# Performance work log

Measured on AMD Instinct MI355X. Metric: run time of the kernel, lower is better.

## Reference

```python
import jax, jax.numpy as jnp
import numpy as np

N, E, D, L = 50000, 600000, 128, 3
EPS = 1e-5


def _layer_norm(x, g, b):
    m = jnp.mean(x, axis=-1, keepdims=True)
    v = jnp.mean((x - m) ** 2, axis=-1, keepdims=True)
    return (x - m) * jax.lax.rsqrt(v + EPS) * g + b


def setup_inputs() -> dict:
    key = jax.random.key(0)
    ks = jax.random.split(key, 20)
    s = 1.0 / np.sqrt(D)
    inp = {
        "node": jax.random.normal(ks[0], (N, D), jnp.float32),
        "edge_attr": jax.random.uniform(ks[1], (E,), jnp.float32),
        # stacked per-layer parameters [L, ...]
        "W_rel": jax.random.uniform(ks[2], (L, D, D), jnp.float32, -s, s),
        "b_rel": jax.random.uniform(ks[3], (L, D), jnp.float32, -s, s),
        "W_root": jax.random.uniform(ks[4], (L, D, D), jnp.float32, -s, s),
        "ln1_g": jnp.ones((L, D), jnp.float32),
        "ln1_b": jnp.zeros((L, D), jnp.float32),
        "ln2_g": jnp.ones((L, D), jnp.float32),
        "ln2_b": jnp.zeros((L, D), jnp.float32),
        "W1": jax.random.uniform(ks[5], (L, D, D), jnp.float32, -s, s),
        "b1": jax.random.uniform(ks[6], (L, D), jnp.float32, -s, s),
        "W2": jax.random.uniform(ks[7], (L, D, D), jnp.float32, -s, s),
        "b2": jax.random.uniform(ks[8], (L, D), jnp.float32, -s, s),
        "jk_W": jax.random.uniform(ks[9], (L * D, D), jnp.float32, -1.0 / np.sqrt(L * D), 1.0 / np.sqrt(L * D)),
        "jk_b": jax.random.uniform(ks[10], (D,), jnp.float32, -1.0 / np.sqrt(L * D), 1.0 / np.sqrt(L * D)),
        "edge_index": jax.random.randint(ks[11], (2, E), 0, N, jnp.int64),
        "batch_ptr": jnp.sort(jax.random.randint(ks[12], (51,), 0, N, jnp.int64)),
    }
    return inp


def reference(node, edge_attr, W_rel, b_rel, W_root, ln1_g, ln1_b, ln2_g, ln2_b,
              W1, b1, W2, b2, jk_W, jk_b, edge_index, batch_ptr):
    src, dst = edge_index[0], edge_index[1]
    deg = jax.ops.segment_sum(jnp.ones((E,), node.dtype), dst, num_segments=N)
    inv_deg = 1.0 / jnp.maximum(deg, 1.0)  # nodes with no in-edges -> 0 aggregate
    outs = []
    for l in range(L):
        msg = node[src] * edge_attr[:, None]                       # [E, D] gather
        agg = jax.ops.segment_sum(msg, dst, num_segments=N)        # scatter-sum
        mean = agg * inv_deg[:, None]                              # mean aggregation
        # GraphConv: lin_rel(aggr) + lin_root(x); skip_connection=False
        node = mean @ W_rel[l] + b_rel[l] + node @ W_root[l]
        node = jax.nn.relu(_layer_norm(node @ W1[l] + b1[l], ln1_g[l], ln1_b[l]))
        node = jax.nn.relu(_layer_norm(node @ W2[l] + b2[l], ln2_g[l], ln2_b[l]))
        outs.append(node)
    jk = jnp.concatenate(outs, axis=-1)                            # [N, L*D]
    return jk @ jk_W + jk_b
```

## Files before the change

### kernel.cpp

```cpp
#include <hip/hip_runtime.h>

#define NN 50000
#define EE 600000
#define DD 128
#define CAP 64
#define BINS 196
#define NP (BINS * 256)
#define BINCAP 3584
#define BCSTRIDE 16
#define LDS_STRIDE 136
#define P1_EDGES 2048
#define P1_BLOCKS ((EE + P1_EDGES - 1) / P1_EDGES)

typedef __attribute__((ext_vector_type(8))) short bf16x8;
typedef __attribute__((ext_vector_type(4))) float f32x4;

__device__ __forceinline__ unsigned short f2bf(float f) {
    union { float f; unsigned u; } v; v.f = f;
    unsigned r = v.u + 0x7FFF + ((v.u >> 16) & 1);
    return (unsigned short)(r >> 16);
}
__device__ __forceinline__ float bflo(unsigned x) { return __uint_as_float(x << 16); }
__device__ __forceinline__ float bfhi(unsigned x) { return __uint_as_float(x & 0xffff0000u); }

__global__ __launch_bounds__(256) void fill_p1(
    const int* __restrict__ src, const int* __restrict__ dst, const float* __restrict__ ea,
    int* __restrict__ binCnt, unsigned long long* __restrict__ recs) {
    __shared__ int hist[BINS];
    __shared__ int lstart[BINS];
    __shared__ int gbase[BINS];
    __shared__ int scan[256];
    __shared__ unsigned long long srt[P1_EDGES];
    const int t = threadIdx.x;
    for (int i = t; i < BINS; i += 256) hist[i] = 0;
    __syncthreads();

    unsigned long long rec[8];
    int bin[8], rnk[8];
    bool val[8];
#pragma unroll
    for (int g = 0; g < 2; ++g) {
        int e0 = blockIdx.x * P1_EDGES + g * 1024 + t * 4;
        int4 dv, sv; float4 ev;
        if (e0 + 3 < EE) {
            dv = *(const int4*)&dst[e0];
            sv = *(const int4*)&src[e0];
            ev = *(const float4*)&ea[e0];
        } else {
            int* dp = (int*)&dv; int* sp = (int*)&sv; float* ep = (float*)&ev;
#pragma unroll
            for (int k = 0; k < 4; ++k) {
                int e = e0 + k;
                dp[k] = (e < EE) ? dst[e] : 0;
                sp[k] = (e < EE) ? src[e] : 0;
                ep[k] = (e < EE) ? ea[e] : 0.f;
            }
        }
#pragma unroll
        for (int k = 0; k < 4; ++k) {
            int i = g * 4 + k;
            int e = e0 + k;
            val[i] = (e < EE);
            int d = ((const int*)&dv)[k];
            unsigned w16 = (unsigned)__float2int_rn(((const float*)&ev)[k] * 65535.0f);
            if (w16 > 65535u) w16 = 65535u;
            rec[i] = ((unsigned long long)(unsigned)d << 32) |
                     (((unsigned)((const int*)&sv)[k]) << 16) | w16;
            bin[i] = d >> 8;
            rnk[i] = val[i] ? atomicAdd(&hist[bin[i]], 1) : 0;
        }
    }
    __syncthreads();
    scan[t] = (t < BINS) ? hist[t] : 0;
    __syncthreads();
#pragma unroll
    for (int off = 1; off < 256; off <<= 1) {
        int v = (t >= off) ? scan[t - off] : 0;
        __syncthreads();
        scan[t] += v;
        __syncthreads();
    }
    if (t < BINS) {
        lstart[t] = scan[t] - hist[t];
        gbase[t] = hist[t] ? atomicAdd(&binCnt[t * BCSTRIDE], hist[t]) : 0;
    }
    __syncthreads();
#pragma unroll
    for (int i = 0; i < 8; ++i)
        if (val[i]) srt[lstart[bin[i]] + rnk[i]] = rec[i];
    __syncthreads();
    const int total = scan[255];
    for (int j = t; j < total; j += 256) {
        unsigned long long r = srt[j];
        int b = (int)(r >> 40);
        int o = gbase[b] + (j - lstart[b]);
        if (o < BINCAP) recs[(size_t)b * BINCAP + o] = r;
    }
}

__global__ __launch_bounds__(256) void fill_p2(
    const int* __restrict__ binCnt, const unsigned long long* __restrict__ recs,
    int* __restrict__ cnt, unsigned* __restrict__ slots) {
    __shared__ int cl[128];
    __shared__ unsigned sl[128 * CAP];
    const int b = blockIdx.x >> 1, half = blockIdx.x & 1, t = threadIdx.x;
    if (t < 128) cl[t] = 0;
    __syncthreads();
    int n = binCnt[b * BCSTRIDE];
    if (n > BINCAP) n = BINCAP;
    const unsigned long long* rp = recs + (size_t)b * BINCAP;
    for (int j = t; j < n; j += 256) {
        unsigned long long r = rp[j];
        int dl = (int)(r >> 32) & 255;
        if ((dl >> 7) == half) {
            int p = atomicAdd(&cl[dl & 127], 1);
            if (p < CAP) sl[(dl & 127) * CAP + p] = (unsigned)r;
        }
    }
    __syncthreads();
    const int node0 = (b << 8) + (half << 7);
    if (t < 128) cnt[node0 + t] = cl[t];
    const uint4* s4 = (const uint4*)sl;
    uint4* g4 = (uint4*)(slots + (size_t)node0 * CAP);
    for (int i = t; i < 2048; i += 256) g4[i] = s4[i];
}

#define CONV_BLKS 6250
__global__ void prep_kernel(const float* __restrict__ nodef, unsigned short* __restrict__ node_bf,
                            const float* __restrict__ W_rel, const float* __restrict__ W_root,
                            const float* __restrict__ W1, const float* __restrict__ W2,
                            const float* __restrict__ jkW,
                            const float* __restrict__ b_rel, const float* __restrict__ b1,
                            float* __restrict__ bc, unsigned short* __restrict__ packed) {
    int b = blockIdx.x;
    if (b < 96) {
        int tg = b * 256 + threadIdx.x;
        int chunk = tg >> 11, r = tg & 2047;
        int lane = r & 63, tile = r >> 6;
        int kt = tile >> 3, nt = tile & 7;
        int quad = lane >> 4, n = lane & 15;
        int k0 = kt * 32 + quad * 8;
        int col = nt * 16 + n;
        union { unsigned short u[8]; uint4 v; } tmp;
        if (chunk < 6) {
            int l = (chunk < 3) ? chunk : chunk - 3;
            const float* A = ((chunk < 3) ? W_rel : W_root) + (size_t)l * 16384;
            const float* B = W1 + (size_t)l * 16384;
            float acc[8] = {0.f, 0.f, 0.f, 0.f, 0.f, 0.f, 0.f, 0.f};
            for (int k = 0; k < 128; ++k) {
                float bv = B[k * 128 + col];
#pragma unroll
                for (int j = 0; j < 8; ++j) acc[j] = fmaf(A[(k0 + j) * 128 + k], bv, acc[j]);
            }
#pragma unroll
            for (int j = 0; j < 8; ++j) tmp.u[j] = f2bf(acc[j]);
        } else {
            const float* s = (chunk < 9) ? (W2 + (size_t)(chunk - 6) * 16384)
                                         : (jkW + (size_t)(chunk - 9) * 16384);
#pragma unroll
            for (int j = 0; j < 8; ++j) tmp.u[j] = f2bf(s[(size_t)(k0 + j) * DD + col]);
        }
        *(uint4*)&packed[(size_t)tg * 8] = tmp.v;
    } else if (b == 96) {
        for (int o = threadIdx.x; o < 384; o += 256) {
            int l = o >> 7, j = o & 127;
            float s = 0.f;
            for (int k = 0; k < 128; ++k)
                s = fmaf(b_rel[l * 128 + k], W1[(size_t)l * 16384 + k * 128 + j], s);
            bc[o] = s + b1[o];
        }
    } else {
        int i = (b - 97) * 256 + threadIdx.x;
        float4 v = *(const float4*)&nodef[(size_t)i * 4];
        ushort4 o;
        o.x = f2bf(v.x); o.y = f2bf(v.y); o.z = f2bf(v.z); o.w = f2bf(v.w);
        *(ushort4*)&node_bf[(size_t)i * 4] = o;
    }
}

template <bool JK>
__global__ __launch_bounds__(64, 4) void fused_layer(
    const unsigned short* __restrict__ feat,
    const unsigned* __restrict__ slots, const int* __restrict__ cnt,
    const unsigned short* __restrict__ PWrel, const unsigned short* __restrict__ PWroot,
    const unsigned short* __restrict__ PW2,
    const float* __restrict__ bc, const float* __restrict__ ln1g, const float* __restrict__ ln1b,
    const float* __restrict__ b2, const float* __restrict__ ln2g, const float* __restrict__ ln2b,
    unsigned short* __restrict__ out,
    const unsigned short* __restrict__ o0, const unsigned short* __restrict__ o1,
    const unsigned short* __restrict__ PJ0, const unsigned short* __restrict__ PJ1,
    const unsigned short* __restrict__ PJ2,
    const float* __restrict__ jkb, float* __restrict__ fout) {
    __shared__ __align__(16) unsigned short wt[16 * LDS_STRIDE];
    const int lane = threadIdx.x;
    const int mrow = blockIdx.x * 16;
    const int quad = lane >> 4, n15 = lane & 15;
    const int kq   = quad * 8;

    {
        const int g4 = lane >> 4;
        const int i8 = n15 * 8;
        const float wscale = 1.0f / 65535.0f;
#pragma unroll
        for (int j4 = 0; j4 < 16; j4 += 4) {
            const int node = mrow + j4 + g4;
            int c = cnt[node];
            if (c > CAP) c = CAP;
            const unsigned* sp = slots + (size_t)node * CAP;
            float acc[8] = {0.f, 0.f, 0.f, 0.f, 0.f, 0.f, 0.f, 0.f};
            for (int j0 = 0; j0 < c; j0 += 4) {
                uint4 sv = *(const uint4*)&sp[j0];
                unsigned se[4] = {sv.x, sv.y, sv.z, sv.w};
#pragma unroll
                for (int t = 0; t < 4; ++t) {
                    bool ok = (j0 + t) < c;
                    unsigned e = se[t];
                    int   srcn = ok ? (int)(e >> 16) : 0;
                    float w    = ok ? (float)(e & 0xffffu) * wscale : 0.0f;
                    uint4 v = *(const uint4*)&feat[(size_t)srcn * DD + i8];
                    acc[0] = fmaf(bflo(v.x), w, acc[0]);
                    acc[1] = fmaf(bfhi(v.x), w, acc[1]);
                    acc[2] = fmaf(bflo(v.y), w, acc[2]);
                    acc[3] = fmaf(bfhi(v.y), w, acc[3]);
                    acc[4] = fmaf(bflo(v.z), w, acc[4]);
                    acc[5] = fmaf(bfhi(v.z), w, acc[5]);
                    acc[6] = fmaf(bflo(v.w), w, acc[6]);
                    acc[7] = fmaf(bfhi(v.w), w, acc[7]);
                }
            }
            float id = 1.0f / fmaxf((float)c, 1.0f);
            union { unsigned short u[8]; uint4 v; } o;
#pragma unroll
            for (int k = 0; k < 8; ++k) o.u[k] = f2bf(acc[k] * id);
            *(uint4*)&wt[(j4 + g4) * LDS_STRIDE + i8] = o.v;
        }
    }
    __asm__ __volatile__("s_waitcnt lgkmcnt(0)" ::: "memory");

    const unsigned short* An = feat + (size_t)(mrow + n15) * DD;

    f32x4 acc[8];
#pragma unroll
    for (int nt = 0; nt < 8; ++nt) acc[nt] = (f32x4){0.f, 0.f, 0.f, 0.f};
#pragma unroll
    for (int kt = 0; kt < 4; ++kt) {
        bf16x8 am = *(const bf16x8*)&wt[n15 * LDS_STRIDE + kt * 32 + kq];
        bf16x8 an = *(const bf16x8*)&An[kt * 32 + kq];
#pragma unroll
        for (int nt = 0; nt < 8; ++nt) {
            bf16x8 brel = *(const bf16x8*)&PWrel[(size_t)((kt * 8 + nt) * 64 + lane) * 8];
            acc[nt] = __builtin_amdgcn_mfma_f32_16x16x32_bf16(am, brel, acc[nt], 0, 0, 0);
            bf16x8 brt = *(const bf16x8*)&PWroot[(size_t)((kt * 8 + nt) * 64 + lane) * 8];
            acc[nt] = __builtin_amdgcn_mfma_f32_16x16x32_bf16(an, brt, acc[nt], 0, 0, 0);
        }
    }

    float x[8][4];
#pragma unroll
    for (int nt = 0; nt < 8; ++nt) {
        float bv = bc[nt * 16 + n15];
#pragma unroll
        for (int r = 0; r < 4; ++r) x[nt][r] = acc[nt][r] + bv;
    }
    {
        float s[4] = {0, 0, 0, 0}, q[4] = {0, 0, 0, 0};
#pragma unroll
        for (int nt = 0; nt < 8; ++nt)
#pragma unroll
            for (int r = 0; r < 4; ++r) { s[r] += x[nt][r]; q[r] += x[nt][r] * x[nt][r]; }
#pragma unroll
        for (int m = 1; m <= 8; m <<= 1)
#pragma unroll
            for (int r = 0; r < 4; ++r) { s[r] += __shfl_xor(s[r], m); q[r] += __shfl_xor(q[r], m); }
        const float inv = 1.0f / 128.0f;
#pragma unroll
        for (int r = 0; r < 4; ++r) {
            float mu = s[r] * inv;
            float rs = rsqrtf(fmaxf(q[r] * inv - mu * mu, 0.0f) + 1e-5f);
#pragma unroll
            for (int nt = 0; nt < 8; ++nt) {
                float g = ln1g[nt * 16 + n15], bb = ln1b[nt * 16 + n15];
                x[nt][r] = fmaxf((x[nt][r] - mu) * rs * g + bb, 0.0f);
            }
        }
    }

#pragma unroll
    for (int nt = 0; nt < 8; ++nt)
#pragma unroll
        for (int r = 0; r < 4; ++r)
            wt[(quad * 4 + r) * LDS_STRIDE + nt * 16 + n15] = f2bf(x[nt][r]);
    __asm__ __volatile__("s_waitcnt lgkmcnt(0)" ::: "memory");

    f32x4 acc2[8];
#pragma unroll
    for (int nt = 0; nt < 8; ++nt) acc2[nt] = (f32x4){0.f, 0.f, 0.f, 0.f};
#pragma unroll
    for (int kt = 0; kt < 4; ++kt) {
        bf16x8 ah = *(const bf16x8*)&wt[n15 * LDS_STRIDE + kt * 32 + kq];
#pragma unroll
        for (int nt = 0; nt < 8; ++nt) {
            bf16x8 bw = *(const bf16x8*)&PW2[(size_t)((kt * 8 + nt) * 64 + lane) * 8];
            acc2[nt] = __builtin_amdgcn_mfma_f32_16x16x32_bf16(ah, bw, acc2[nt], 0, 0, 0);
        }
    }
#pragma unroll
    for (int nt = 0; nt < 8; ++nt) {
        float bv = b2[nt * 16 + n15];
#pragma unroll
        for (int r = 0; r < 4; ++r) x[nt][r] = acc2[nt][r] + bv;
    }
    {
        float s[4] = {0, 0, 0, 0}, q[4] = {0, 0, 0, 0};
#pragma unroll
        for (int nt = 0; nt < 8; ++nt)
#pragma unroll
            for (int r = 0; r < 4; ++r) { s[r] += x[nt][r]; q[r] += x[nt][r] * x[nt][r]; }
#pragma unroll
        for (int m = 1; m <= 8; m <<= 1)
#pragma unroll
            for (int r = 0; r < 4; ++r) { s[r] += __shfl_xor(s[r], m); q[r] += __shfl_xor(q[r], m); }
        const float inv = 1.0f / 128.0f;
#pragma unroll
        for (int r = 0; r < 4; ++r) {
            float mu = s[r] * inv;
            float rs = rsqrtf(fmaxf(q[r] * inv - mu * mu, 0.0f) + 1e-5f);
#pragma unroll
            for (int nt = 0; nt < 8; ++nt) {
                float g = ln2g[nt * 16 + n15], bb = ln2b[nt * 16 + n15];
                x[nt][r] = fmaxf((x[nt][r] - mu) * rs * g + bb, 0.0f);
            }
        }
    }

    __asm__ __volatile__("s_waitcnt lgkmcnt(0)" ::: "memory");
#pragma unroll
    for (int nt = 0; nt < 8; ++nt)
#pragma unroll
        for (int r = 0; r < 4; ++r)
            wt[(quad * 4 + r) * LDS_STRIDE + nt * 16 + n15] = f2bf(x[nt][r]);
    __asm__ __volatile__("s_waitcnt lgkmcnt(0)" ::: "memory");

    if constexpr (!JK) {
#pragma unroll
        for (int i = 0; i < 4; ++i) {
            int s = i * 512 + lane * 8;
            int r = s >> 7, col = s & 127;
            uint4 v = *(const uint4*)&wt[r * LDS_STRIDE + col];
            *(uint4*)&out[(size_t)(mrow + r) * DD + col] = v;
        }
    } else {
        f32x4 accJ[8];
#pragma unroll
        for (int nt = 0; nt < 8; ++nt) accJ[nt] = (f32x4){0.f, 0.f, 0.f, 0.f};
#pragma unroll
        for (int kt = 0; kt < 4; ++kt) {
            bf16x8 ah = *(const bf16x8*)&wt[n15 * LDS_STRIDE + kt * 32 + kq];
#pragma unroll
            for (int nt = 0; nt < 8; ++nt) {
                bf16x8 bw = *(const bf16x8*)&PJ2[(size_t)((kt * 8 + nt) * 64 + lane) * 8];
                accJ[nt] = __builtin_amdgcn_mfma_f32_16x16x32_bf16(ah, bw, accJ[nt], 0, 0, 0);
            }
        }
        const unsigned short* A0 = o0 + (size_t)(mrow + n15) * DD;
        const unsigned short* A1 = o1 + (size_t)(mrow + n15) * DD;
#pragma unroll
        for (int kt = 0; kt < 4; ++kt) {
            bf16x8 a0 = *(const bf16x8*)&A0[kt * 32 + kq];
            bf16x8 a1 = *(const bf16x8*)&A1[kt * 32 + kq];
#pragma unroll
            for (int nt = 0; nt < 8; ++nt) {
                bf16x8 b0 = *(const bf16x8*)&PJ0[(size_t)((kt * 8 + nt) * 64 + lane) * 8];
                accJ[nt] = __builtin_amdgcn_mfma_f32_16x16x32_bf16(a0, b0, accJ[nt], 0, 0, 0);
                bf16x8 b1 = *(const bf16x8*)&PJ1[(size_t)((kt * 8 + nt) * 64 + lane) * 8];
                accJ[nt] = __builtin_amdgcn_mfma_f32_16x16x32_bf16(a1, b1, accJ[nt], 0, 0, 0);
            }
        }
#pragma unroll
        for (int nt = 0; nt < 8; ++nt) {
            float bv = jkb[nt * 16 + n15];
#pragma unroll
            for (int r = 0; r < 4; ++r)
                fout[(size_t)(mrow + quad * 4 + r) * DD + nt * 16 + n15] = accJ[nt][r] + bv;
        }
    }
}

extern "C" void kernel_launch(void* const* d_in, const int* in_sizes, int n_in,
                              void* d_out, int out_size, void* d_ws, size_t ws_size,
                              hipStream_t stream) {
    const float* node   = (const float*)d_in[0];
    const float* ea     = (const float*)d_in[1];
    const float* W_rel  = (const float*)d_in[2];
    const float* b_rel  = (const float*)d_in[3];
    const float* W_root = (const float*)d_in[4];
    const float* ln1_g  = (const float*)d_in[5];
    const float* ln1_b  = (const float*)d_in[6];
    const float* ln2_g  = (const float*)d_in[7];
    const float* ln2_b  = (const float*)d_in[8];
    const float* W1     = (const float*)d_in[9];
    const float* b1     = (const float*)d_in[10];
    const float* W2     = (const float*)d_in[11];
    const float* b2     = (const float*)d_in[12];
    const float* jk_W   = (const float*)d_in[13];
    const float* jk_b   = (const float*)d_in[14];
    const int*   ei     = (const int*)d_in[15];
    const int* srcI = ei;
    const int* dstI = ei + EE;

    char* ws = (char*)d_ws;
    size_t off = 0;
    auto alloc = [&](size_t bytes) {
        void* p = ws + off;
        off += (bytes + 255) & ~(size_t)255;
        return p;
    };
    int*                binCnt  = (int*)alloc((size_t)BINS * BCSTRIDE * 4);
    unsigned long long* recs    = (unsigned long long*)alloc((size_t)BINS * BINCAP * 8);
    int*                cnt     = (int*)alloc((size_t)NP * 4);
    unsigned*           slots   = (unsigned*)alloc((size_t)NP * CAP * 4);
    unsigned short*     node_bf = (unsigned short*)alloc((size_t)NN * DD * 2);
    unsigned short* outs_bf[2];
    for (int l = 0; l < 2; ++l) outs_bf[l] = (unsigned short*)alloc((size_t)NN * DD * 2);
    float*              bc      = (float*)alloc((size_t)3 * 128 * 4);
    unsigned short*     packed  = (unsigned short*)alloc((size_t)12 * 16384 * 2);

    hipMemsetAsync(binCnt, 0, (size_t)BINS * BCSTRIDE * 4, stream);
    fill_p1<<<P1_BLOCKS, 256, 0, stream>>>(srcI, dstI, ea, binCnt, recs);
    fill_p2<<<BINS * 2, 256, 0, stream>>>(binCnt, recs, cnt, slots);
    prep_kernel<<<97 + CONV_BLKS, 256, 0, stream>>>(
        node, node_bf, W_rel, W_root, W1, W2, jk_W, b_rel, b1, bc, packed);

    const int gblocks = NN / 16;
    unsigned short* cur = node_bf;
    for (int l = 0; l < 3; ++l) {
        if (l < 2) {
            fused_layer<false><<<gblocks, 64, 0, stream>>>(
                cur, slots, cnt,
                packed + (size_t)l * 16384, packed + (size_t)(3 + l) * 16384,
                packed + (size_t)(6 + l) * 16384,
                bc + (size_t)l * DD, ln1_g + (size_t)l * DD, ln1_b + (size_t)l * DD,
                b2 + (size_t)l * DD, ln2_g + (size_t)l * DD, ln2_b + (size_t)l * DD,
                outs_bf[l],
                nullptr, nullptr, nullptr, nullptr, nullptr, nullptr, nullptr);
            cur = outs_bf[l];
        } else {
            fused_layer<true><<<gblocks, 64, 0, stream>>>(
                cur, slots, cnt,
                packed + (size_t)l * 16384, packed + (size_t)(3 + l) * 16384,
                packed + (size_t)(6 + l) * 16384,
                bc + (size_t)l * DD, ln1_g + (size_t)l * DD, ln1_b + (size_t)l * DD,
                b2 + (size_t)l * DD, ln2_g + (size_t)l * DD, ln2_b + (size_t)l * DD,
                nullptr,
                outs_bf[0], outs_bf[1],
                packed + (size_t)9 * 16384, packed + (size_t)10 * 16384, packed + (size_t)11 * 16384,
                jk_b, (float*)d_out);
        }
    }
}
```

Baseline: 265.0 us.

## Split fused layer across four waves per 16-row block

Each block of 16 nodes now runs with 256 threads instead of one wave. The four waves each aggregate 4 rows of the gather and own 2 of the 8 output column tiles in each GEMM. LayerNorm statistics are combined across waves through a small shared buffer, and barriers replace the single-wave LDS waits. The goal is more parallelism and fewer registers per wave for the latency-bound gather, at the cost of extra __syncthreads and a cross-wave reduction.

New measurement: 282.7 us. 6.7% more time.

```diff
diff --git a/kernel.cpp b/kernel.cpp
--- a/kernel.cpp
+++ b/kernel.cpp
@@ -179,7 +179,7 @@
 }
 
 template <bool JK>
-__global__ __launch_bounds__(64, 4) void fused_layer(
+__global__ __launch_bounds__(256, 8) void fused_layer(
     const unsigned short* __restrict__ feat,
     const unsigned* __restrict__ slots, const int* __restrict__ cnt,
     const unsigned short* __restrict__ PWrel, const unsigned short* __restrict__ PWroot,
@@ -192,174 +192,193 @@
     const unsigned short* __restrict__ PJ2,
     const float* __restrict__ jkb, float* __restrict__ fout) {
     __shared__ __align__(16) unsigned short wt[16 * LDS_STRIDE];
-    const int lane = threadIdx.x;
+    __shared__ float lnbuf[4][16][2];
+    const int tid  = threadIdx.x;
+    const int wv   = tid >> 6;
+    const int lane = tid & 63;
     const int mrow = blockIdx.x * 16;
     const int quad = lane >> 4, n15 = lane & 15;
     const int kq   = quad * 8;
 
     {
-        const int g4 = lane >> 4;
-        const int i8 = n15 * 8;
+        const int i8  = n15 * 8;
+        const int row = wv * 4 + quad;
+        const int node = mrow + row;
+        int c = cnt[node];
+        if (c > CAP) c = CAP;
+        const unsigned* sp = slots + (size_t)node * CAP;
+        float acc[8] = {0.f, 0.f, 0.f, 0.f, 0.f, 0.f, 0.f, 0.f};
         const float wscale = 1.0f / 65535.0f;
-#pragma unroll
-        for (int j4 = 0; j4 < 16; j4 += 4) {
-            const int node = mrow + j4 + g4;
-            int c = cnt[node];
-            if (c > CAP) c = CAP;
-            const unsigned* sp = slots + (size_t)node * CAP;
-            float acc[8] = {0.f, 0.f, 0.f, 0.f, 0.f, 0.f, 0.f, 0.f};
-            for (int j0 = 0; j0 < c; j0 += 4) {
-                uint4 sv = *(const uint4*)&sp[j0];
-                unsigned se[4] = {sv.x, sv.y, sv.z, sv.w};
-#pragma unroll
-                for (int t = 0; t < 4; ++t) {
-                    bool ok = (j0 + t) < c;
-                    unsigned e = se[t];
-                    int   srcn = ok ? (int)(e >> 16) : 0;
-                    float w    = ok ? (float)(e & 0xffffu) * wscale : 0.0f;
-                    uint4 v = *(const uint4*)&feat[(size_t)srcn * DD + i8];
-                    acc[0] = fmaf(bflo(v.x), w, acc[0]);
-                    acc[1] = fmaf(bfhi(v.x), w, acc[1]);
-                    acc[2] = fmaf(bflo(v.y), w, acc[2]);
-                    acc[3] = fmaf(bfhi(v.y), w, acc[3]);
-                    acc[4] = fmaf(bflo(v.z), w, acc[4]);
-                    acc[5] = fmaf(bfhi(v.z), w, acc[5]);
-                    acc[6] = fmaf(bflo(v.w), w, acc[6]);
-                    acc[7] = fmaf(bfhi(v.w), w, acc[7]);
-                }
-            }
-            float id = 1.0f / fmaxf((float)c, 1.0f);
-            union { unsigned short u[8]; uint4 v; } o;
-#pragma unroll
-            for (int k = 0; k < 8; ++k) o.u[k] = f2bf(acc[k] * id);
-            *(uint4*)&wt[(j4 + g4) * LDS_STRIDE + i8] = o.v;
-        }
-    }
-    __asm__ __volatile__("s_waitcnt lgkmcnt(0)" ::: "memory");
+        for (int j0 = 0; j0 < c; j0 += 4) {
+            uint4 sv = *(const uint4*)&sp[j0];
+            unsigned se[4] = {sv.x, sv.y, sv.z, sv.w};
+#pragma unroll
+            for (int t = 0; t < 4; ++t) {
+                bool ok = (j0 + t) < c;
+                unsigned e = se[t];
+                int   srcn = ok ? (int)(e >> 16) : 0;
+                float w    = ok ? (float)(e & 0xffffu) * wscale : 0.0f;
+                uint4 v = *(const uint4*)&feat[(size_t)srcn * DD + i8];
+                acc[0] = fmaf(bflo(v.x), w, acc[0]);
+                acc[1] = fmaf(bfhi(v.x), w, acc[1]);
+                acc[2] = fmaf(bflo(v.y), w, acc[2]);
+                acc[3] = fmaf(bfhi(v.y), w, acc[3]);
+                acc[4] = fmaf(bflo(v.z), w, acc[4]);
+                acc[5] = fmaf(bfhi(v.z), w, acc[5]);
+                acc[6] = fmaf(bflo(v.w), w, acc[6]);
+                acc[7] = fmaf(bfhi(v.w), w, acc[7]);
+            }
+        }
+        float id = 1.0f / fmaxf((float)c, 1.0f);
+        union { unsigned short u[8]; uint4 v; } o;
+#pragma unroll
+        for (int k = 0; k < 8; ++k) o.u[k] = f2bf(acc[k] * id);
+        *(uint4*)&wt[row * LDS_STRIDE + i8] = o.v;
+    }
+    __syncthreads();
 
     const unsigned short* An = feat + (size_t)(mrow + n15) * DD;
 
-    f32x4 acc[8];
-#pragma unroll
-    for (int nt = 0; nt < 8; ++nt) acc[nt] = (f32x4){0.f, 0.f, 0.f, 0.f};
+    const int nt0 = wv * 2;
+    f32x4 acc1[2];
+    acc1[0] = (f32x4){0.f, 0.f, 0.f, 0.f};
+    acc1[1] = (f32x4){0.f, 0.f, 0.f, 0.f};
 #pragma unroll
     for (int kt = 0; kt < 4; ++kt) {
         bf16x8 am = *(const bf16x8*)&wt[n15 * LDS_STRIDE + kt * 32 + kq];
         bf16x8 an = *(const bf16x8*)&An[kt * 32 + kq];
 #pragma unroll
-        for (int nt = 0; nt < 8; ++nt) {
+        for (int ntl = 0; ntl < 2; ++ntl) {
+            int nt = nt0 + ntl;
             bf16x8 brel = *(const bf16x8*)&PWrel[(size_t)((kt * 8 + nt) * 64 + lane) * 8];
-            acc[nt] = __builtin_amdgcn_mfma_f32_16x16x32_bf16(am, brel, acc[nt], 0, 0, 0);
+            acc1[ntl] = __builtin_amdgcn_mfma_f32_16x16x32_bf16(am, brel, acc1[ntl], 0, 0, 0);
             bf16x8 brt = *(const bf16x8*)&PWroot[(size_t)((kt * 8 + nt) * 64 + lane) * 8];
-            acc[nt] = __builtin_amdgcn_mfma_f32_16x16x32_bf16(an, brt, acc[nt], 0, 0, 0);
-        }
-    }
-
-    float x[8][4];
-#pragma unroll
-    for (int nt = 0; nt < 8; ++nt) {
-        float bv = bc[nt * 16 + n15];
-#pragma unroll
-        for (int r = 0; r < 4; ++r) x[nt][r] = acc[nt][r] + bv;
+            acc1[ntl] = __builtin_amdgcn_mfma_f32_16x16x32_bf16(an, brt, acc1[ntl], 0, 0, 0);
+        }
+    }
+
+    float x[2][4];
+#pragma unroll
+    for (int ntl = 0; ntl < 2; ++ntl) {
+        float bv = bc[(nt0 + ntl) * 16 + n15];
+#pragma unroll
+        for (int r = 0; r < 4; ++r) x[ntl][r] = acc1[ntl][r] + bv;
     }
     {
-        float s[4] = {0, 0, 0, 0}, q[4] = {0, 0, 0, 0};
-#pragma unroll
-        for (int nt = 0; nt < 8; ++nt)
-#pragma unroll
-            for (int r = 0; r < 4; ++r) { s[r] += x[nt][r]; q[r] += x[nt][r] * x[nt][r]; }
+        float s[4], q[4];
+#pragma unroll
+        for (int r = 0; r < 4; ++r) {
+            s[r] = x[0][r] + x[1][r];
+            q[r] = x[0][r] * x[0][r] + x[1][r] * x[1][r];
+        }
 #pragma unroll
         for (int m = 1; m <= 8; m <<= 1)
 #pragma unroll
             for (int r = 0; r < 4; ++r) { s[r] += __shfl_xor(s[r], m); q[r] += __shfl_xor(q[r], m); }
+        if (n15 == 0) {
+#pragma unroll
+            for (int r = 0; r < 4; ++r) {
+                lnbuf[wv][quad * 4 + r][0] = s[r];
+                lnbuf[wv][quad * 4 + r][1] = q[r];
+            }
+        }
+        __syncthreads();
         const float inv = 1.0f / 128.0f;
 #pragma unroll
         for (int r = 0; r < 4; ++r) {
-            float mu = s[r] * inv;
-            float rs = rsqrtf(fmaxf(q[r] * inv - mu * mu, 0.0f) + 1e-5f);
-#pragma unroll
-            for (int nt = 0; nt < 8; ++nt) {
-                float g = ln1g[nt * 16 + n15], bb = ln1b[nt * 16 + n15];
-                x[nt][r] = fmaxf((x[nt][r] - mu) * rs * g + bb, 0.0f);
-            }
-        }
-    }
-
-#pragma unroll
-    for (int nt = 0; nt < 8; ++nt)
+            int row = quad * 4 + r;
+            float sf = lnbuf[0][row][0] + lnbuf[1][row][0] + lnbuf[2][row][0] + lnbuf[3][row][0];
+            float qf = lnbuf[0][row][1] + lnbuf[1][row][1] + lnbuf[2][row][1] + lnbuf[3][row][1];
+            float mu = sf * inv;
+            float rs = rsqrtf(fmaxf(qf * inv - mu * mu, 0.0f) + 1e-5f);
+#pragma unroll
+            for (int ntl = 0; ntl < 2; ++ntl) {
+                float g = ln1g[(nt0 + ntl) * 16 + n15], bb = ln1b[(nt0 + ntl) * 16 + n15];
+                x[ntl][r] = fmaxf((x[ntl][r] - mu) * rs * g + bb, 0.0f);
+            }
+        }
+    }
+#pragma unroll
+    for (int ntl = 0; ntl < 2; ++ntl)
 #pragma unroll
         for (int r = 0; r < 4; ++r)
-            wt[(quad * 4 + r) * LDS_STRIDE + nt * 16 + n15] = f2bf(x[nt][r]);
-    __asm__ __volatile__("s_waitcnt lgkmcnt(0)" ::: "memory");
-
-    f32x4 acc2[8];
-#pragma unroll
-    for (int nt = 0; nt < 8; ++nt) acc2[nt] = (f32x4){0.f, 0.f, 0.f, 0.f};
+            wt[(quad * 4 + r) * LDS_STRIDE + (nt0 + ntl) * 16 + n15] = f2bf(x[ntl][r]);
+    __syncthreads();
+
+    f32x4 acc2[2];
+    acc2[0] = (f32x4){0.f, 0.f, 0.f, 0.f};
+    acc2[1] = (f32x4){0.f, 0.f, 0.f, 0.f};
 #pragma unroll
     for (int kt = 0; kt < 4; ++kt) {
         bf16x8 ah = *(const bf16x8*)&wt[n15 * LDS_STRIDE + kt * 32 + kq];
 #pragma unroll
-        for (int nt = 0; nt < 8; ++nt) {
-            bf16x8 bw = *(const bf16x8*)&PW2[(size_t)((kt * 8 + nt) * 64 + lane) * 8];
-            acc2[nt] = __builtin_amdgcn_mfma_f32_16x16x32_bf16(ah, bw, acc2[nt], 0, 0, 0);
-        }
-    }
-#pragma unroll
-    for (int nt = 0; nt < 8; ++nt) {
-        float bv = b2[nt * 16 + n15];
-#pragma unroll
-        for (int r = 0; r < 4; ++r) x[nt][r] = acc2[nt][r] + bv;
+        for (int ntl = 0; ntl < 2; ++ntl) {
+            bf16x8 bw = *(const bf16x8*)&PW2[(size_t)((kt * 8 + nt0 + ntl) * 64 + lane) * 8];
+            acc2[ntl] = __builtin_amdgcn_mfma_f32_16x16x32_bf16(ah, bw, acc2[ntl], 0, 0, 0);
+        }
+    }
+#pragma unroll
+    for (int ntl = 0; ntl < 2; ++ntl) {
+        float bv = b2[(nt0 + ntl) * 16 + n15];
+#pragma unroll
+        for (int r = 0; r < 4; ++r) x[ntl][r] = acc2[ntl][r] + bv;
     }
     {
-        float s[4] = {0, 0, 0, 0}, q[4] = {0, 0, 0, 0};
-#pragma unroll
-        for (int nt = 0; nt < 8; ++nt)
-#pragma unroll
-            for (int r = 0; r < 4; ++r) { s[r] += x[nt][r]; q[r] += x[nt][r] * x[nt][r]; }
+        float s[4], q[4];
+#pragma unroll
+        for (int r = 0; r < 4; ++r) {
+            s[r] = x[0][r] + x[1][r];
+            q[r] = x[0][r] * x[0][r] + x[1][r] * x[1][r];
+        }
 #pragma unroll
         for (int m = 1; m <= 8; m <<= 1)
 #pragma unroll
             for (int r = 0; r < 4; ++r) { s[r] += __shfl_xor(s[r], m); q[r] += __shfl_xor(q[r], m); }
+        if (n15 == 0) {
+#pragma unroll
+            for (int r = 0; r < 4; ++r) {
+                lnbuf[wv][quad * 4 + r][0] = s[r];
+                lnbuf[wv][quad * 4 + r][1] = q[r];
+            }
+        }
+        __syncthreads();
         const float inv = 1.0f / 128.0f;
 #pragma unroll
         for (int r = 0; r < 4; ++r) {
-            float mu = s[r] * inv;
-            float rs = rsqrtf(fmaxf(q[r] * inv - mu * mu, 0.0f) + 1e-5f);
-#pragma unroll
-            for (int nt = 0; nt < 8; ++nt) {
-                float g = ln2g[nt * 16 + n15], bb = ln2b[nt * 16 + n15];
-                x[nt][r] = fmaxf((x[nt][r] - mu) * rs * g + bb, 0.0f);
-            }
-        }
-    }
-
-    __asm__ __volatile__("s_waitcnt lgkmcnt(0)" ::: "memory");
-#pragma unroll
-    for (int nt = 0; nt < 8; ++nt)
+            int row = quad * 4 + r;
+            float sf = lnbuf[0][row][0] + lnbuf[1][row][0] + lnbuf[2][row][0] + lnbuf[3][row][0];
+            float qf = lnbuf[0][row][1] + lnbuf[1][row][1] + lnbuf[2][row][1] + lnbuf[3][row][1];
+            float mu = sf * inv;
+            float rs = rsqrtf(fmaxf(qf * inv - mu * mu, 0.0f) + 1e-5f);
+#pragma unroll
+            for (int ntl = 0; ntl < 2; ++ntl) {
+                float g = ln2g[(nt0 + ntl) * 16 + n15], bb = ln2b[(nt0 + ntl) * 16 + n15];
+                x[ntl][r] = fmaxf((x[ntl][r] - mu) * rs * g + bb, 0.0f);
+            }
+        }
+    }
+#pragma unroll
+    for (int ntl = 0; ntl < 2; ++ntl)
 #pragma unroll
         for (int r = 0; r < 4; ++r)
-            wt[(quad * 4 + r) * LDS_STRIDE + nt * 16 + n15] = f2bf(x[nt][r]);
-    __asm__ __volatile__("s_waitcnt lgkmcnt(0)" ::: "memory");
+            wt[(quad * 4 + r) * LDS_STRIDE + (nt0 + ntl) * 16 + n15] = f2bf(x[ntl][r]);
+    __syncthreads();
 
     if constexpr (!JK) {
-#pragma unroll
-        for (int i = 0; i < 4; ++i) {
-            int s = i * 512 + lane * 8;
-            int r = s >> 7, col = s & 127;
-            uint4 v = *(const uint4*)&wt[r * LDS_STRIDE + col];
-            *(uint4*)&out[(size_t)(mrow + r) * DD + col] = v;
-        }
+        int r = tid >> 4, col = (tid & 15) * 8;
+        uint4 v = *(const uint4*)&wt[r * LDS_STRIDE + col];
+        *(uint4*)&out[(size_t)(mrow + r) * DD + col] = v;
     } else {
-        f32x4 accJ[8];
-#pragma unroll
-        for (int nt = 0; nt < 8; ++nt) accJ[nt] = (f32x4){0.f, 0.f, 0.f, 0.f};
+        f32x4 accJ[2];
+        accJ[0] = (f32x4){0.f, 0.f, 0.f, 0.f};
+        accJ[1] = (f32x4){0.f, 0.f, 0.f, 0.f};
 #pragma unroll
         for (int kt = 0; kt < 4; ++kt) {
             bf16x8 ah = *(const bf16x8*)&wt[n15 * LDS_STRIDE + kt * 32 + kq];
 #pragma unroll
-            for (int nt = 0; nt < 8; ++nt) {
-                bf16x8 bw = *(const bf16x8*)&PJ2[(size_t)((kt * 8 + nt) * 64 + lane) * 8];
-                accJ[nt] = __builtin_amdgcn_mfma_f32_16x16x32_bf16(ah, bw, accJ[nt], 0, 0, 0);
+            for (int ntl = 0; ntl < 2; ++ntl) {
+                bf16x8 bw = *(const bf16x8*)&PJ2[(size_t)((kt * 8 + nt0 + ntl) * 64 + lane) * 8];
+                accJ[ntl] = __builtin_amdgcn_mfma_f32_16x16x32_bf16(ah, bw, accJ[ntl], 0, 0, 0);
             }
         }
         const unsigned short* A0 = o0 + (size_t)(mrow + n15) * DD;
@@ -369,19 +388,19 @@
             bf16x8 a0 = *(const bf16x8*)&A0[kt * 32 + kq];
             bf16x8 a1 = *(const bf16x8*)&A1[kt * 32 + kq];
 #pragma unroll
-            for (int nt = 0; nt < 8; ++nt) {
-                bf16x8 b0 = *(const bf16x8*)&PJ0[(size_t)((kt * 8 + nt) * 64 + lane) * 8];
-                accJ[nt] = __builtin_amdgcn_mfma_f32_16x16x32_bf16(a0, b0, accJ[nt], 0, 0, 0);
-                bf16x8 b1 = *(const bf16x8*)&PJ1[(size_t)((kt * 8 + nt) * 64 + lane) * 8];
-                accJ[nt] = __builtin_amdgcn_mfma_f32_16x16x32_bf16(a1, b1, accJ[nt], 0, 0, 0);
-            }
-        }
-#pragma unroll
-        for (int nt = 0; nt < 8; ++nt) {
-            float bv = jkb[nt * 16 + n15];
+            for (int ntl = 0; ntl < 2; ++ntl) {
+                bf16x8 b0 = *(const bf16x8*)&PJ0[(size_t)((kt * 8 + nt0 + ntl) * 64 + lane) * 8];
+                accJ[ntl] = __builtin_amdgcn_mfma_f32_16x16x32_bf16(a0, b0, accJ[ntl], 0, 0, 0);
+                bf16x8 b1 = *(const bf16x8*)&PJ1[(size_t)((kt * 8 + nt0 + ntl) * 64 + lane) * 8];
+                accJ[ntl] = __builtin_amdgcn_mfma_f32_16x16x32_bf16(a1, b1, accJ[ntl], 0, 0, 0);
+            }
+        }
+#pragma unroll
+        for (int ntl = 0; ntl < 2; ++ntl) {
+            float bv = jkb[(nt0 + ntl) * 16 + n15];
 #pragma unroll
             for (int r = 0; r < 4; ++r)
-                fout[(size_t)(mrow + quad * 4 + r) * DD + nt * 16 + n15] = accJ[nt][r] + bv;
+                fout[(size_t)(mrow + quad * 4 + r) * DD + (nt0 + ntl) * 16 + n15] = accJ[ntl][r] + bv;
         }
     }
 }
@@ -435,7 +454,7 @@
     unsigned short* cur = node_bf;
     for (int l = 0; l < 3; ++l) {
         if (l < 2) {
-            fused_layer<false><<<gblocks, 64, 0, stream>>>(
+            fused_layer<false><<<gblocks, 256, 0, stream>>>(
                 cur, slots, cnt,
                 packed + (size_t)l * 16384, packed + (size_t)(3 + l) * 16384,
                 packed + (size_t)(6 + l) * 16384,
@@ -445,7 +464,7 @@
                 nullptr, nullptr, nullptr, nullptr, nullptr, nullptr, nullptr);
             cur = outs_bf[l];
         } else {
-            fused_layer<true><<<gblocks, 64, 0, stream>>>(
+            fused_layer<true><<<gblocks, 256, 0, stream>>>(
                 cur, slots, cnt,
                 packed + (size_t)l * 16384, packed + (size_t)(3 + l) * 16384,
                 packed + (size_t)(6 + l) * 16384,
```

## Software-pipeline neighbor gathers, hoist root loads, fold bin-count memset into prep

Applied to the files above, without the earlier changes.

The aggregation loop now issues the next group of four neighbor feature loads before accumulating the current group, so gather latency overlaps with the FMAs. Neighbor counts are loaded once per lane and broadcast with shuffles, and the root-feature MFMA operands are loaded up front before aggregation starts. The separate memset of the bin counters is removed and folded into the prep kernel, which now launches before the fill kernels. The cost is higher register pressure from the double-buffered gather registers, which could reduce occupancy.

Measured after the change: 260.3 us. No clear change (-1.8%).

```diff
diff --git a/kernel.cpp b/kernel.cpp
--- a/kernel.cpp
+++ b/kernel.cpp
@@ -131,7 +131,8 @@
                             const float* __restrict__ W1, const float* __restrict__ W2,
                             const float* __restrict__ jkW,
                             const float* __restrict__ b_rel, const float* __restrict__ b1,
-                            float* __restrict__ bc, unsigned short* __restrict__ packed) {
+                            float* __restrict__ bc, unsigned short* __restrict__ packed,
+                            int* __restrict__ binCnt) {
     int b = blockIdx.x;
     if (b < 96) {
         int tg = b * 256 + threadIdx.x;
@@ -162,6 +163,7 @@
         }
         *(uint4*)&packed[(size_t)tg * 8] = tmp.v;
     } else if (b == 96) {
+        if (threadIdx.x < BINS) binCnt[threadIdx.x * BCSTRIDE] = 0;
         for (int o = threadIdx.x; o < 384; o += 256) {
             int l = o >> 7, j = o & 127;
             float s = 0.f;
@@ -196,48 +198,71 @@
     const int mrow = blockIdx.x * 16;
     const int quad = lane >> 4, n15 = lane & 15;
     const int kq   = quad * 8;
-
-    {
-        const int g4 = lane >> 4;
-        const int i8 = n15 * 8;
-        const float wscale = 1.0f / 65535.0f;
-#pragma unroll
-        for (int j4 = 0; j4 < 16; j4 += 4) {
-            const int node = mrow + j4 + g4;
-            int c = cnt[node];
-            if (c > CAP) c = CAP;
-            const unsigned* sp = slots + (size_t)node * CAP;
-            float acc[8] = {0.f, 0.f, 0.f, 0.f, 0.f, 0.f, 0.f, 0.f};
-            for (int j0 = 0; j0 < c; j0 += 4) {
-                uint4 sv = *(const uint4*)&sp[j0];
-                unsigned se[4] = {sv.x, sv.y, sv.z, sv.w};
-#pragma unroll
-                for (int t = 0; t < 4; ++t) {
-                    bool ok = (j0 + t) < c;
-                    unsigned e = se[t];
-                    int   srcn = ok ? (int)(e >> 16) : 0;
-                    float w    = ok ? (float)(e & 0xffffu) * wscale : 0.0f;
-                    uint4 v = *(const uint4*)&feat[(size_t)srcn * DD + i8];
-                    acc[0] = fmaf(bflo(v.x), w, acc[0]);
-                    acc[1] = fmaf(bfhi(v.x), w, acc[1]);
-                    acc[2] = fmaf(bflo(v.y), w, acc[2]);
-                    acc[3] = fmaf(bfhi(v.y), w, acc[3]);
-                    acc[4] = fmaf(bflo(v.z), w, acc[4]);
-                    acc[5] = fmaf(bfhi(v.z), w, acc[5]);
-                    acc[6] = fmaf(bflo(v.w), w, acc[6]);
-                    acc[7] = fmaf(bfhi(v.w), w, acc[7]);
-                }
-            }
-            float id = 1.0f / fmaxf((float)c, 1.0f);
-            union { unsigned short u[8]; uint4 v; } o;
-#pragma unroll
-            for (int k = 0; k < 8; ++k) o.u[k] = f2bf(acc[k] * id);
-            *(uint4*)&wt[(j4 + g4) * LDS_STRIDE + i8] = o.v;
-        }
+    const int i8   = n15 * 8;
+    const float wscale = 1.0f / 65535.0f;
+
+    const int cl0 = cnt[mrow + n15];
+    const int cAll = (cl0 > CAP) ? CAP : cl0;
+
+    const unsigned short* An = feat + (size_t)(mrow + n15) * DD;
+    bf16x8 an4[4];
+#pragma unroll
+    for (int kt = 0; kt < 4; ++kt) an4[kt] = *(const bf16x8*)&An[kt * 32 + kq];
+
+#pragma unroll
+    for (int r = 0; r < 4; ++r) {
+        const int row = r * 4 + quad;
+        int c = __shfl(cAll, row);
+        const unsigned* sp = slots + (size_t)(mrow + row) * CAP;
+        float acc[8] = {0.f, 0.f, 0.f, 0.f, 0.f, 0.f, 0.f, 0.f};
+        uint4 sv = *(const uint4*)&sp[0];
+        unsigned ec[4] = {sv.x, sv.y, sv.z, sv.w};
+        int   s[4]; float w[4]; uint4 f[4];
+#pragma unroll
+        for (int tt = 0; tt < 4; ++tt) {
+            bool ok = tt < c;
+            s[tt] = ok ? (int)(ec[tt] >> 16) : 0;
+            w[tt] = ok ? (float)(ec[tt] & 0xffffu) * wscale : 0.0f;
+        }
+#pragma unroll
+        for (int tt = 0; tt < 4; ++tt)
+            f[tt] = *(const uint4*)&feat[(size_t)s[tt] * DD + i8];
+
+        for (int j0 = 0; j0 < c; j0 += 4) {
+            const int jn = j0 + 4;
+            uint4 svn = *(const uint4*)&sp[(jn < c) ? jn : 0];
+            unsigned en[4] = {svn.x, svn.y, svn.z, svn.w};
+            int ns[4]; float nw[4]; uint4 g[4];
+#pragma unroll
+            for (int tt = 0; tt < 4; ++tt) {
+                bool ok = (jn + tt) < c;
+                ns[tt] = ok ? (int)(en[tt] >> 16) : 0;
+                nw[tt] = ok ? (float)(en[tt] & 0xffffu) * wscale : 0.0f;
+            }
+#pragma unroll
+            for (int tt = 0; tt < 4; ++tt)
+                g[tt] = *(const uint4*)&feat[(size_t)ns[tt] * DD + i8];
+#pragma unroll
+            for (int tt = 0; tt < 4; ++tt) {
+                acc[0] = fmaf(bflo(f[tt].x), w[tt], acc[0]);
+                acc[1] = fmaf(bfhi(f[tt].x), w[tt], acc[1]);
+                acc[2] = fmaf(bflo(f[tt].y), w[tt], acc[2]);
+                acc[3] = fmaf(bfhi(f[tt].y), w[tt], acc[3]);
+                acc[4] = fmaf(bflo(f[tt].z), w[tt], acc[4]);
+                acc[5] = fmaf(bfhi(f[tt].z), w[tt], acc[5]);
+                acc[6] = fmaf(bflo(f[tt].w), w[tt], acc[6]);
+                acc[7] = fmaf(bfhi(f[tt].w), w[tt], acc[7]);
+            }
+#pragma unroll
+            for (int tt = 0; tt < 4; ++tt) { f[tt] = g[tt]; w[tt] = nw[tt]; }
+        }
+        float id = 1.0f / fmaxf((float)c, 1.0f);
+        union { unsigned short u[8]; uint4 v; } o;
+#pragma unroll
+        for (int k = 0; k < 8; ++k) o.u[k] = f2bf(acc[k] * id);
+        *(uint4*)&wt[row * LDS_STRIDE + i8] = o.v;
     }
     __asm__ __volatile__("s_waitcnt lgkmcnt(0)" ::: "memory");
-
-    const unsigned short* An = feat + (size_t)(mrow + n15) * DD;
 
     f32x4 acc[8];
 #pragma unroll
@@ -245,13 +270,12 @@
 #pragma unroll
     for (int kt = 0; kt < 4; ++kt) {
         bf16x8 am = *(const bf16x8*)&wt[n15 * LDS_STRIDE + kt * 32 + kq];
-        bf16x8 an = *(const bf16x8*)&An[kt * 32 + kq];
 #pragma unroll
         for (int nt = 0; nt < 8; ++nt) {
             bf16x8 brel = *(const bf16x8*)&PWrel[(size_t)((kt * 8 + nt) * 64 + lane) * 8];
             acc[nt] = __builtin_amdgcn_mfma_f32_16x16x32_bf16(am, brel, acc[nt], 0, 0, 0);
             bf16x8 brt = *(const bf16x8*)&PWroot[(size_t)((kt * 8 + nt) * 64 + lane) * 8];
-            acc[nt] = __builtin_amdgcn_mfma_f32_16x16x32_bf16(an, brt, acc[nt], 0, 0, 0);
+            acc[nt] = __builtin_amdgcn_mfma_f32_16x16x32_bf16(an4[kt], brt, acc[nt], 0, 0, 0);
         }
     }
 
@@ -425,11 +449,10 @@
     float*              bc      = (float*)alloc((size_t)3 * 128 * 4);
     unsigned short*     packed  = (unsigned short*)alloc((size_t)12 * 16384 * 2);
 
-    hipMemsetAsync(binCnt, 0, (size_t)BINS * BCSTRIDE * 4, stream);
+    prep_kernel<<<97 + CONV_BLKS, 256, 0, stream>>>(
+        node, node_bf, W_rel, W_root, W1, W2, jk_W, b_rel, b1, bc, packed, binCnt);
     fill_p1<<<P1_BLOCKS, 256, 0, stream>>>(srcI, dstI, ea, binCnt, recs);
     fill_p2<<<BINS * 2, 256, 0, stream>>>(binCnt, recs, cnt, slots);
-    prep_kernel<<<97 + CONV_BLKS, 256, 0, stream>>>(
-        node, node_bf, W_rel, W_root, W1, W2, jk_W, b_rel, b1, bc, packed);
 
     const int gblocks = NN / 16;
     unsigned short* cur = node_bf;
```

## Stage slot lists in LDS, prefetch root operands, fold memset into prep kernel

Applied to the files above, without the earlier changes.

The fused layer kernel now loads the 16 nodes' slot lists cooperatively into LDS with coalesced 16-byte loads, broadcasts per-node counts with shuffles, and issues the root-operand loads before the gather loop so their latency overlaps it. The binCnt zeroing moves from a separate memset into prep_kernel, which now runs before fill_p1, removing one launch. The gather loop now reads per-node edge records from LDS instead of global memory. Extra LDS and registers for the prefetched operands may reduce occupancy.

Measured after the change: 258.8 us. 1.02x faster.

```diff
diff --git a/kernel.cpp b/kernel.cpp
--- a/kernel.cpp
+++ b/kernel.cpp
@@ -4,6 +4,7 @@
 #define EE 600000
 #define DD 128
 #define CAP 64
+#define SLDS_STRIDE 66
 #define BINS 196
 #define NP (BINS * 256)
 #define BINCAP 3584
@@ -131,7 +132,8 @@
                             const float* __restrict__ W1, const float* __restrict__ W2,
                             const float* __restrict__ jkW,
                             const float* __restrict__ b_rel, const float* __restrict__ b1,
-                            float* __restrict__ bc, unsigned short* __restrict__ packed) {
+                            float* __restrict__ bc, unsigned short* __restrict__ packed,
+                            int* __restrict__ binCnt) {
     int b = blockIdx.x;
     if (b < 96) {
         int tg = b * 256 + threadIdx.x;
@@ -162,6 +164,7 @@
         }
         *(uint4*)&packed[(size_t)tg * 8] = tmp.v;
     } else if (b == 96) {
+        if (threadIdx.x < BINS) binCnt[threadIdx.x * BCSTRIDE] = 0;
         for (int o = threadIdx.x; o < 384; o += 256) {
             int l = o >> 7, j = o & 127;
             float s = 0.f;
@@ -192,52 +195,67 @@
     const unsigned short* __restrict__ PJ2,
     const float* __restrict__ jkb, float* __restrict__ fout) {
     __shared__ __align__(16) unsigned short wt[16 * LDS_STRIDE];
+    __shared__ __align__(16) unsigned slds[16 * SLDS_STRIDE];
     const int lane = threadIdx.x;
     const int mrow = blockIdx.x * 16;
     const int quad = lane >> 4, n15 = lane & 15;
     const int kq   = quad * 8;
+    const int i8   = n15 * 8;
+    const float wscale = 1.0f / 65535.0f;
+
+    const int cl0 = cnt[mrow + n15];
+    const int cAll = (cl0 > CAP) ? CAP : cl0;
 
     {
-        const int g4 = lane >> 4;
-        const int i8 = n15 * 8;
-        const float wscale = 1.0f / 65535.0f;
-#pragma unroll
-        for (int j4 = 0; j4 < 16; j4 += 4) {
-            const int node = mrow + j4 + g4;
-            int c = cnt[node];
-            if (c > CAP) c = CAP;
-            const unsigned* sp = slots + (size_t)node * CAP;
-            float acc[8] = {0.f, 0.f, 0.f, 0.f, 0.f, 0.f, 0.f, 0.f};
-            for (int j0 = 0; j0 < c; j0 += 4) {
-                uint4 sv = *(const uint4*)&sp[j0];
-                unsigned se[4] = {sv.x, sv.y, sv.z, sv.w};
-#pragma unroll
-                for (int t = 0; t < 4; ++t) {
-                    bool ok = (j0 + t) < c;
-                    unsigned e = se[t];
-                    int   srcn = ok ? (int)(e >> 16) : 0;
-                    float w    = ok ? (float)(e & 0xffffu) * wscale : 0.0f;
-                    uint4 v = *(const uint4*)&feat[(size_t)srcn * DD + i8];
-                    acc[0] = fmaf(bflo(v.x), w, acc[0]);
-                    acc[1] = fmaf(bfhi(v.x), w, acc[1]);
-                    acc[2] = fmaf(bflo(v.y), w, acc[2]);
-                    acc[3] = fmaf(bfhi(v.y), w, acc[3]);
-                    acc[4] = fmaf(bflo(v.z), w, acc[4]);
-                    acc[5] = fmaf(bfhi(v.z), w, acc[5]);
-                    acc[6] = fmaf(bflo(v.w), w, acc[6]);
-                    acc[7] = fmaf(bfhi(v.w), w, acc[7]);
-                }
-            }
-            float id = 1.0f / fmaxf((float)c, 1.0f);
-            union { unsigned short u[8]; uint4 v; } o;
-#pragma unroll
-            for (int k = 0; k < 8; ++k) o.u[k] = f2bf(acc[k] * id);
-            *(uint4*)&wt[(j4 + g4) * LDS_STRIDE + i8] = o.v;
-        }
-    }
+        const unsigned* sbase = slots + (size_t)mrow * CAP;
+#pragma unroll
+        for (int k = 0; k < 4; ++k) {
+            int li = k * 64 + lane;
+            uint4 v = *(const uint4*)&sbase[li * 4];
+            int rw = li >> 4, cu = (li & 15) * 4;
+            *(uint4*)&slds[rw * SLDS_STRIDE + cu] = v;
+        }
+    }
+
+    const unsigned short* An = feat + (size_t)(mrow + n15) * DD;
+    bf16x8 an4[4];
+#pragma unroll
+    for (int kt = 0; kt < 4; ++kt) an4[kt] = *(const bf16x8*)&An[kt * 32 + kq];
+
     __asm__ __volatile__("s_waitcnt lgkmcnt(0)" ::: "memory");
 
-    const unsigned short* An = feat + (size_t)(mrow + n15) * DD;
+#pragma unroll
+    for (int r = 0; r < 4; ++r) {
+        const int row = r * 4 + quad;
+        int c = __shfl(cAll, row);
+        float acc[8] = {0.f, 0.f, 0.f, 0.f, 0.f, 0.f, 0.f, 0.f};
+        for (int j0 = 0; j0 < c; j0 += 4) {
+            uint4 sv = *(const uint4*)&slds[row * SLDS_STRIDE + j0];
+            unsigned se[4] = {sv.x, sv.y, sv.z, sv.w};
+#pragma unroll
+            for (int tt = 0; tt < 4; ++tt) {
+                bool ok = (j0 + tt) < c;
+                unsigned e = se[tt];
+                int   srcn = ok ? (int)(e >> 16) : 0;
+                float w    = ok ? (float)(e & 0xffffu) * wscale : 0.0f;
+                uint4 v = *(const uint4*)&feat[(size_t)srcn * DD + i8];
+                acc[0] = fmaf(bflo(v.x), w, acc[0]);
+                acc[1] = fmaf(bfhi(v.x), w, acc[1]);
+                acc[2] = fmaf(bflo(v.y), w, acc[2]);
+                acc[3] = fmaf(bfhi(v.y), w, acc[3]);
+                acc[4] = fmaf(bflo(v.z), w, acc[4]);
+                acc[5] = fmaf(bfhi(v.z), w, acc[5]);
+                acc[6] = fmaf(bflo(v.w), w, acc[6]);
+                acc[7] = fmaf(bfhi(v.w), w, acc[7]);
+            }
+        }
+        float id = 1.0f / fmaxf((float)c, 1.0f);
+        union { unsigned short u[8]; uint4 v; } o;
+#pragma unroll
+        for (int k = 0; k < 8; ++k) o.u[k] = f2bf(acc[k] * id);
+        *(uint4*)&wt[row * LDS_STRIDE + i8] = o.v;
+    }
+    __asm__ __volatile__("s_waitcnt lgkmcnt(0)" ::: "memory");
 
     f32x4 acc[8];
 #pragma unroll
@@ -245,13 +263,12 @@
 #pragma unroll
     for (int kt = 0; kt < 4; ++kt) {
         bf16x8 am = *(const bf16x8*)&wt[n15 * LDS_STRIDE + kt * 32 + kq];
-        bf16x8 an = *(const bf16x8*)&An[kt * 32 + kq];
 #pragma unroll
         for (int nt = 0; nt < 8; ++nt) {
             bf16x8 brel = *(const bf16x8*)&PWrel[(size_t)((kt * 8 + nt) * 64 + lane) * 8];
             acc[nt] = __builtin_amdgcn_mfma_f32_16x16x32_bf16(am, brel, acc[nt], 0, 0, 0);
             bf16x8 brt = *(const bf16x8*)&PWroot[(size_t)((kt * 8 + nt) * 64 + lane) * 8];
-            acc[nt] = __builtin_amdgcn_mfma_f32_16x16x32_bf16(an, brt, acc[nt], 0, 0, 0);
+            acc[nt] = __builtin_amdgcn_mfma_f32_16x16x32_bf16(an4[kt], brt, acc[nt], 0, 0, 0);
         }
     }
 
@@ -425,11 +442,10 @@
     float*              bc      = (float*)alloc((size_t)3 * 128 * 4);
     unsigned short*     packed  = (unsigned short*)alloc((size_t)12 * 16384 * 2);
 
-    hipMemsetAsync(binCnt, 0, (size_t)BINS * BCSTRIDE * 4, stream);
+    prep_kernel<<<97 + CONV_BLKS, 256, 0, stream>>>(
+        node, node_bf, W_rel, W_root, W1, W2, jk_W, b_rel, b1, bc, packed, binCnt);
     fill_p1<<<P1_BLOCKS, 256, 0, stream>>>(srcI, dstI, ea, binCnt, recs);
     fill_p2<<<BINS * 2, 256, 0, stream>>>(binCnt, recs, cnt, slots);
-    prep_kernel<<<97 + CONV_BLKS, 256, 0, stream>>>(
-        node, node_bf, W_rel, W_root, W1, W2, jk_W, b_rel, b1, bc, packed);
 
     const int gblocks = NN / 16;
     unsigned short* cur = node_bf;
```
